# Kernel optimization log

Hardware: AMD Instinct MI355X
Metric: run time of the kernel (lower is better)

The kernel has to match this reference:

```python
import jax, jax.numpy as jnp
import numpy as np

# dims
R, K, N, V = 2, 3, 16384, 256          # r_len, num feat keys, nodes, raw feat dim
E, L, VE = 1, 8, 128                   # num extra keys, extra seq len, extra raw dim
LK, OUT = 1, 64                        # num label keys, out_feats (num classes)
IN, HID = 256, 512                     # in_feats, hidden
C = K + E + LK                         # num_channels for grouped conv / LayerNorm
LN_EPS = 1e-5


def _xav(key, shape, fan_in, fan_out):
    s = np.sqrt(2.0 / (fan_in + fan_out)).astype(np.float32)
    return jax.random.normal(key, shape, dtype=jnp.float32) * s


def setup_inputs() -> dict:
    key = jax.random.key(0)
    ks = jax.random.split(key, 16)
    inp = {}
    # forward args (dict-of-tensor structures flattened to stacked arrays in sorted-key order)
    inp["raw_feats"] = jax.random.normal(ks[0], (R, K, N, V), dtype=jnp.float32)
    inp["extra_feats"] = jax.random.normal(ks[1], (R, E, N, L, VE), dtype=jnp.float32)
    inp["label_feats"] = jax.random.normal(ks[2], (R, LK, N, OUT), dtype=jnp.float32)
    # per-relation embedding tables (original: uniform(-0.5,0.5); scaled for numeric tameness)
    inp["feat_emb"] = jax.random.uniform(ks[3], (R, K, V, IN), minval=-0.05, maxval=0.05, dtype=jnp.float32)
    inp["extra_emb"] = jax.random.uniform(ks[4], (R, E, VE, IN), minval=-0.05, maxval=0.05, dtype=jnp.float32)
    inp["label_emb"] = jax.random.uniform(ks[5], (R, LK, OUT, IN), minval=-0.05, maxval=0.05, dtype=jnp.float32)
    # sigmoid-attention weight vectors
    inp["w_extra"] = _xav(ks[6], (E, IN), IN, 1)      # embed_weight_r_extra
    inp["w_r"] = _xav(ks[7], (R, HID), HID, 1)        # embed_weight_r
    inp["w_global"] = _xav(ks[8], (HID,), HID, 1)     # self.w
    # grouped conv1x1 stack + LayerNorm([C,HID]) + PReLU (x2)
    inp["W1"] = _xav(ks[9], (C, IN, HID), IN, HID)
    inp["b1"] = jnp.zeros((C, HID), jnp.float32)
    inp["g1"] = jnp.ones((C, HID), jnp.float32)
    inp["be1"] = jnp.zeros((C, HID), jnp.float32)
    inp["a1"] = jnp.float32(0.25)
    inp["W2"] = _xav(ks[10], (C, HID, HID), HID, HID)
    inp["b2"] = jnp.zeros((C, HID), jnp.float32)
    inp["g2"] = jnp.ones((C, HID), jnp.float32)
    inp["be2"] = jnp.zeros((C, HID), jnp.float32)
    inp["a2"] = jnp.float32(0.25)
    # FeedForwardNet (n_layers_2 = 2)
    inp["Wf1"] = _xav(ks[11], (HID, HID), HID, HID)
    inp["bf1"] = jnp.zeros((HID,), jnp.float32)
    inp["af"] = jnp.float32(0.25)
    inp["Wf2"] = _xav(ks[12], (HID, OUT), HID, OUT)
    inp["bf2"] = jnp.zeros((OUT,), jnp.float32)
    return inp


def _prelu(x, a):
    return jnp.where(x >= 0, x, a * x)


def _ln(x, g, b):
    # LayerNorm over last two dims ([C, HID]) as in nn.LayerNorm([num_channels, hidden])
    m = jnp.mean(x, axis=(-2, -1), keepdims=True)
    v = jnp.var(x, axis=(-2, -1), keepdims=True)
    return (x - m) * jax.lax.rsqrt(v + LN_EPS) * g + b


def _attn_pool(f, w):
    # f: [N, C, D], w: [D] -> softmax(sigmoid(f @ w)) over C, weighted sum -> [N, D]
    gv = jax.nn.softmax(jax.nn.sigmoid(f @ w), axis=-1)
    return jnp.einsum('ncd,nc->nd', f, gv)


def reference(raw_feats, extra_feats, label_feats, feat_emb, extra_emb, label_emb,
              w_extra, w_r, w_global, W1, b1, g1, be1, a1, W2, b2, g2, be2, a2,
              Wf1, bf1, af, Wf2, bf2):
    outs = []
    for r in range(R):  # small fixed ensemble loop (structurally distinct params)
        mapped = jnp.einsum('knv,kvd->nkd', raw_feats[r], feat_emb[r])        # [N,K,IN]
        me = jnp.einsum('enlv,evd->enld', extra_feats[r], extra_emb[r])       # [E,N,L,IN]
        extra_out = jax.vmap(_attn_pool)(me, w_extra)                          # [E,N,IN]
        ml = jnp.einsum('knc,kcd->nkd', label_feats[r], label_emb[r])         # [N,LK,IN]
        feats = jnp.concatenate([mapped, jnp.moveaxis(extra_out, 0, 1), ml], axis=1)  # [N,C,IN]
        x = jnp.einsum('ncm,cmh->nch', feats, W1) + b1                         # grouped conv1x1
        x = _prelu(_ln(x, g1, be1), a1)
        x = jnp.einsum('nch,chk->nck', x, W2) + b2
        x = _prelu(_ln(x, g2, be2), a2)
        outs.append(_attn_pool(x, w_r[r]))                                     # [N,HID]
    h = jnp.stack(outs, axis=1)                                                # [N,R,HID]
    final = _attn_pool(h, w_global)                                            # [N,HID]
    y = _prelu(final @ Wf1 + bf1, af)
    return y @ Wf2 + bf2
```

## Files before the change

### kernel.cpp

```cpp
#include <hip/hip_runtime.h>


typedef unsigned short bf16_t;
using ushort8v = __attribute__((ext_vector_type(8))) unsigned short;
using bf16x8   = __attribute__((ext_vector_type(8))) __bf16;
using f32x4    = __attribute__((ext_vector_type(4))) float;

#define WAITV(N) asm volatile("s_waitcnt vmcnt(%0)" :: "n"(N) : "memory")
#define WAITL0() asm volatile("s_waitcnt lgkmcnt(0)" ::: "memory")

__device__ __forceinline__ float bf2f(bf16_t u) {
    return __uint_as_float(((unsigned int)u) << 16);
}
__device__ __forceinline__ bf16_t f2bf(float f) {
    unsigned int u = __float_as_uint(f);
    u += 0x7FFFu + ((u >> 16) & 1u);
    return (bf16_t)(u >> 16);
}
__device__ __forceinline__ float ld1(const void* p, long i, int dt) {
    return dt ? bf2f(((const bf16_t*)p)[i]) : ((const float*)p)[i];
}
__device__ __forceinline__ float4 ld4(const void* p, long i, int dt) {
    if (dt) {
        ushort4 v = *(const ushort4*)((const bf16_t*)p + i);
        return make_float4(bf2f(v.x), bf2f(v.y), bf2f(v.z), bf2f(v.w));
    }
    return *(const float4*)((const float*)p + i);
}
__device__ __forceinline__ ushort8v ld8bf(const void* p, long i, int dt) {
    if (dt) return *(const ushort8v*)((const bf16_t*)p + i);
    const float* f = (const float*)p + i;
    float4 a = *(const float4*)f, b = *(const float4*)(f + 4);
    ushort8v r;
    r[0] = f2bf(a.x); r[1] = f2bf(a.y); r[2] = f2bf(a.z); r[3] = f2bf(a.w);
    r[4] = f2bf(b.x); r[5] = f2bf(b.y); r[6] = f2bf(b.z); r[7] = f2bf(b.w);
    return r;
}
__device__ __forceinline__ float decode_scalar(const void* p, int isbf) {
    if (!isbf) return *(const float*)p;
    unsigned int u = *(const unsigned int*)p;
    if ((u & 0xFFFFu) == 0u) return __uint_as_float(u);
    return bf2f((bf16_t)(u & 0xFFFFu));
}
__device__ __forceinline__ float wave_reduce(float v) {
#pragma unroll
    for (int o = 32; o > 0; o >>= 1) v += __shfl_down(v, o, 64);
    return v;
}
__device__ __forceinline__ void gl_lds16(const void* g, void* l) {
    __builtin_amdgcn_global_load_lds(
        (const __attribute__((address_space(1))) void*)g,
        (__attribute__((address_space(3))) void*)l, 16, 0, 0);
}

__global__ void detect_k(const unsigned int* __restrict__ w, long nwords,
                         int* __restrict__ flag)
{
    const int lane = threadIdx.x;
    long idx = (long)lane * 997 + 13;
    if (idx >= nwords) idx = lane % (nwords > 0 ? nwords : 1);
    unsigned int word = w[idx];
    int e = (word >> 7) & 0xFF;
    int vote = (e >= 110 && e <= 134) ? 1 : 0;
    unsigned long long m = __ballot(vote);
    if (lane == 0) *flag = (__popcll(m) >= 32) ? 1 : 0;
}

__global__ __launch_bounds__(256) void transT_k(
    const void* __restrict__ in, long inoff, long sInZ, int Kd, int Nd,
    bf16_t* __restrict__ out, long outoff, long sOutZ,
    const int* __restrict__ flag)
{
    const int isbf = *flag;
    const long z = blockIdx.z;
    long idx = (long)blockIdx.x * 256 + threadIdx.x;
    if (idx >= (long)Kd * Nd) return;
    int k = (int)(idx / Nd), n = (int)(idx % Nd);
    out[outoff + z * sOutZ + (long)n * Kd + k] =
        f2bf(ld1(in, inoff + z * sInZ + idx, isbf));
}

__global__ __launch_bounds__(256) void fold_gemmT_k(
    const void* __restrict__ A, long aoff, long sAz, int lda,
    const void* __restrict__ B, long boff, long sBz, int ldb,
    bf16_t* __restrict__ CT, long coff, long sCz, int ldcT,
    int K, const int* __restrict__ flag)
{
    const int isbf = *flag;
    __shared__ __align__(16) float As[16][68];
    __shared__ __align__(16) float Bs[16][68];
    const int z = blockIdx.z, t = threadIdx.x;
    const int tx = t & 15, ty = t >> 4;
    const int am = t >> 2, ak = (t & 3) << 2;
    const int bn = tx << 2;
    const long aBase = aoff + z * sAz + (long)(blockIdx.y * 64 + am) * lda + ak;
    const long bBase = boff + z * sBz + (long)ty * ldb + blockIdx.x * 64 + bn;
    float acc[4][4] = {};
    for (int k0 = 0; k0 < K; k0 += 16) {
        float4 av = ld4(A, aBase + k0, isbf);
        float4 bv = ld4(B, bBase + (long)k0 * ldb, isbf);
        __syncthreads();
        As[ak + 0][am] = av.x; As[ak + 1][am] = av.y;
        As[ak + 2][am] = av.z; As[ak + 3][am] = av.w;
        *(float4*)&Bs[ty][bn] = bv;
        __syncthreads();
#pragma unroll
        for (int k = 0; k < 16; k++) {
            float4 a4 = *(const float4*)&As[k][ty << 2];
            float4 b4 = *(const float4*)&Bs[k][tx << 2];
            float ar[4] = {a4.x, a4.y, a4.z, a4.w};
            float br[4] = {b4.x, b4.y, b4.z, b4.w};
#pragma unroll
            for (int i = 0; i < 4; i++)
#pragma unroll
                for (int j = 0; j < 4; j++) acc[i][j] += ar[i] * br[j];
        }
    }
    const int cm = blockIdx.y * 64 + (ty << 2);
    const int cn = blockIdx.x * 64 + (tx << 2);
#pragma unroll
    for (int i = 0; i < 4; i++)
#pragma unroll
        for (int j = 0; j < 4; j++)
            CT[coff + z * sCz + (long)(cn + j) * ldcT + (cm + i)] = f2bf(acc[i][j]);
}

template <int BN_, int WNW_, int MODE, int CD>
__global__ __launch_bounds__(256) void mgemm(
    const void* __restrict__ A, int adt, long aoff, long sA1, long sA2, int lda,
    const bf16_t* __restrict__ BT, long boff, long sB1, long sB2,
    void* __restrict__ C, long coff, long sC1, long sC2, int ldc,
    const void* __restrict__ bias, long biasoff, long sBi1, long sBi2,
    const void* __restrict__ alpha_ptr, int K, int zdiv,
    const int* __restrict__ flag)
{
    constexpr int NJ = WNW_ / 16;
    constexpr int BROUNDS = BN_ / 64;
    const int isbf = *flag;
    const int adt_ = (adt == 2) ? isbf : adt;
    const int cdt = (CD == 2) ? isbf : 1;

    __shared__ __align__(16) unsigned short As[3][128 * 32];
    __shared__ __align__(16) unsigned short Bs[3][BN_ * 32];

    const int t = threadIdx.x;
    const int lane = t & 63, w = t >> 6;
    const int quad = lane >> 4, r16 = lane & 15;
    const int wy = w >> 1, wx = w & 1;
    const int z = blockIdx.z;
    const int zq = z / zdiv, zr = z % zdiv;
    const long blockM = (long)blockIdx.y * 128;
    const int  blockN = blockIdx.x * BN_;

    f32x4 acc[4][NJ];
    const f32x4 zero4 = {0.f, 0.f, 0.f, 0.f};
#pragma unroll
    for (int i = 0; i < 4; i++)
#pragma unroll
        for (int j = 0; j < NJ; j++) acc[i][j] = zero4;

    const long aBase = aoff + zq * sA1 + zr * sA2;
    const long bBase = boff + zq * sB1 + zr * sB2;

    const bool fastA = (adt_ == 1);
    const bf16_t* Abf = (const bf16_t*)A;

    auto STAGE = [&](int buf, int ti) {
        const int k0 = ti << 5;
        if (fastA) {
#pragma unroll
            for (int c = 0; c < 2; c++) {
                const int lin = c * 256 + t;
                const int m = lin >> 2, kq = (lin & 3) * 8;
                gl_lds16(Abf + aBase + (blockM + m) * (long)lda + k0 + kq,
                         &As[buf][(size_t)(c * 256 + w * 64) * 8]);
            }
        } else {
            ushort8v av[2];
#pragma unroll
            for (int c = 0; c < 2; c++) {
                const int lin = c * 256 + t;
                const int m = lin >> 2, kq = (lin & 3) * 8;
                av[c] = ld8bf(A, aBase + (blockM + m) * (long)lda + k0 + kq, 0);
            }
#pragma unroll
            for (int c = 0; c < 2; c++)
                *(ushort8v*)&As[buf][(size_t)(c * 256 + t) * 8] = av[c];
        }
#pragma unroll
        for (int c = 0; c < BROUNDS; c++) {
            const int lin = c * 256 + t;
            const int n = lin >> 2, kq = (lin & 3) * 8;
            gl_lds16(BT + bBase + (long)(blockN + n) * K + k0 + kq,
                     &Bs[buf][(size_t)(c * 256 + w * 64) * 8]);
        }
    };

    const int nt = K >> 5;
    STAGE(0, 0);
    if (nt > 1) STAGE(1, 1);

    int cur = 0;
    for (int ti = 0; ti < nt; ++ti) {
        WAITL0();
        if (fastA) {
            if (ti + 1 < nt) WAITV(2 + BROUNDS); else WAITV(0);
        } else {
            if (ti + 1 < nt) WAITV(BROUNDS);     else WAITV(0);
        }
        __builtin_amdgcn_s_barrier();
        __builtin_amdgcn_sched_barrier(0);

        if (ti + 2 < nt) {
            int sb = cur + 2; if (sb >= 3) sb -= 3;
            STAGE(sb, ti + 2);
        }

        bf16x8 af[4], bfr[NJ];
#pragma unroll
        for (int i = 0; i < 4; i++) {
            int m = wy * 64 + i * 16 + r16;
            af[i] = __builtin_bit_cast(bf16x8,
                        *(const ushort8v*)&As[cur][m * 32 + quad * 8]);
        }
#pragma unroll
        for (int j = 0; j < NJ; j++) {
            int n = wx * WNW_ + j * 16 + r16;
            bfr[j] = __builtin_bit_cast(bf16x8,
                        *(const ushort8v*)&Bs[cur][n * 32 + quad * 8]);
        }
#pragma unroll
        for (int i = 0; i < 4; i++)
#pragma unroll
            for (int j = 0; j < NJ; j++)
                acc[i][j] = __builtin_amdgcn_mfma_f32_16x16x32_bf16(
                    af[i], bfr[j], acc[i][j], 0, 0, 0);

        cur = (cur == 2) ? 0 : cur + 1;
    }

    const float alpha = (MODE == 2) ? decode_scalar(alpha_ptr, isbf) : 0.f;
    const long cBase = coff + zq * sC1 + zr * sC2;
#pragma unroll
    for (int j = 0; j < NJ; j++) {
        const int n = blockN + wx * WNW_ + j * 16 + r16;
        const float bz = (MODE >= 1)
            ? ld1(bias, biasoff + zq * sBi1 + zr * sBi2 + n, isbf) : 0.f;
#pragma unroll
        for (int i = 0; i < 4; i++) {
            const long m0 = blockM + wy * 64 + i * 16 + quad * 4;
#pragma unroll
            for (int rg = 0; rg < 4; rg++) {
                float v = acc[i][j][rg] + bz;
                if (MODE == 2) v = (v >= 0.f) ? v : alpha * v;
                const long off = cBase + (m0 + rg) * (long)ldc + n;
                if (cdt) ((bf16_t*)C)[off] = f2bf(v);
                else     ((float*)C)[off] = v;
            }
        }
    }
}

__global__ __launch_bounds__(256) void pool_extra_k(
    const bf16_t* __restrict__ ME, long sMEz, const void* __restrict__ wx,
    float* __restrict__ EO, long sEOz, const int* __restrict__ flag)
{
    const int isbf = *flag;
    const int n = blockIdx.x, t = threadIdx.x;
    const bf16_t* base = ME + blockIdx.y * sMEz + (long)n * 2048;
    float v[8];
#pragma unroll
    for (int l = 0; l < 8; l++) v[l] = bf2f(base[l * 256 + t]);
    const float w = ld1(wx, t, isbf);
    __shared__ float red[8][4];
    const int lane = t & 63, wid = t >> 6;
#pragma unroll
    for (int l = 0; l < 8; l++) {
        float pr = wave_reduce(v[l] * w);
        if (lane == 0) red[l][wid] = pr;
    }
    __syncthreads();
    float gv[8], ssum = 0.f;
#pragma unroll
    for (int l = 0; l < 8; l++) {
        float sc = red[l][0] + red[l][1] + red[l][2] + red[l][3];
        float sg = 1.f / (1.f + expf(-sc));
        float e = expf(sg);
        gv[l] = e; ssum += e;
    }
    const float inv = 1.f / ssum;
    float o = 0.f;
#pragma unroll
    for (int l = 0; l < 8; l++) o += gv[l] * inv * v[l];
    EO[blockIdx.y * sEOz + (long)n * 256 + t] = o;
}

__global__ __launch_bounds__(256) void ln1_k(
    bf16_t* __restrict__ X, const void* __restrict__ g,
    const void* __restrict__ be, const void* __restrict__ alpha_ptr,
    const int* __restrict__ flag)
{
    const int isbf = *flag;
    const int n = blockIdx.x, t = threadIdx.x;
    bf16_t* row = X + (long)n * 2560;
    float v[10], s = 0.f, sq = 0.f;
#pragma unroll
    for (int i = 0; i < 10; i++) {
        float x = bf2f(row[i * 256 + t]);
        v[i] = x; s += x; sq += x * x;
    }
    __shared__ float redS[4], redQ[4];
    const int lane = t & 63, wid = t >> 6;
    float ws_ = wave_reduce(s), wq = wave_reduce(sq);
    if (lane == 0) { redS[wid] = ws_; redQ[wid] = wq; }
    __syncthreads();
    const float S = redS[0] + redS[1] + redS[2] + redS[3];
    const float Q = redQ[0] + redQ[1] + redQ[2] + redQ[3];
    const float mean = S * (1.f / 2560.f);
    const float rstd = rsqrtf(fmaxf(Q * (1.f / 2560.f) - mean * mean, 0.f) + 1e-5f);
    const float alpha = decode_scalar(alpha_ptr, isbf);
#pragma unroll
    for (int i = 0; i < 10; i++) {
        int e = i * 256 + t;
        float y = (v[i] - mean) * rstd * ld1(g, e, isbf) + ld1(be, e, isbf);
        row[e] = f2bf((y >= 0.f) ? y : alpha * y);
    }
}

__global__ __launch_bounds__(256) void ln2_pool_k(
    const bf16_t* __restrict__ X, long sXz, const void* __restrict__ g,
    const void* __restrict__ be, const void* __restrict__ alpha_ptr,
    const void* __restrict__ wr,
    bf16_t* __restrict__ H, const int* __restrict__ flag)
{
    const int isbf = *flag;
    const int n = blockIdx.x, t = threadIdx.x, rr = blockIdx.y;
    const bf16_t* row = X + rr * sXz + (long)n * 2560;
    float v[5][2], s = 0.f, sq = 0.f;
#pragma unroll
    for (int c = 0; c < 5; c++)
#pragma unroll
        for (int hi = 0; hi < 2; hi++) {
            float x = bf2f(row[c * 512 + hi * 256 + t]);
            v[c][hi] = x; s += x; sq += x * x;
        }
    __shared__ float redS[4], redQ[4];
    const int lane = t & 63, wid = t >> 6;
    float ws_ = wave_reduce(s), wq = wave_reduce(sq);
    if (lane == 0) { redS[wid] = ws_; redQ[wid] = wq; }
    __syncthreads();
    const float S = redS[0] + redS[1] + redS[2] + redS[3];
    const float Q = redQ[0] + redQ[1] + redQ[2] + redQ[3];
    const float mean = S * (1.f / 2560.f);
    const float rstd = rsqrtf(fmaxf(Q * (1.f / 2560.f) - mean * mean, 0.f) + 1e-5f);
    const float alpha = decode_scalar(alpha_ptr, isbf);
    const float w0 = ld1(wr, (long)rr * 512 + t, isbf);
    const float w1 = ld1(wr, (long)rr * 512 + t + 256, isbf);
    float p[5];
#pragma unroll
    for (int c = 0; c < 5; c++) {
        p[c] = 0.f;
#pragma unroll
        for (int hi = 0; hi < 2; hi++) {
            int e = c * 512 + hi * 256 + t;
            float y = (v[c][hi] - mean) * rstd * ld1(g, e, isbf) + ld1(be, e, isbf);
            y = (y >= 0.f) ? y : alpha * y;
            v[c][hi] = y;
            p[c] += y * (hi ? w1 : w0);
        }
    }
    __shared__ float redP[5][4];
#pragma unroll
    for (int c = 0; c < 5; c++) {
        float pr = wave_reduce(p[c]);
        if (lane == 0) redP[c][wid] = pr;
    }
    __syncthreads();
    float gv[5], ssum = 0.f;
#pragma unroll
    for (int c = 0; c < 5; c++) {
        float sc = redP[c][0] + redP[c][1] + redP[c][2] + redP[c][3];
        float sg = 1.f / (1.f + expf(-sc));
        float e = expf(sg);
        gv[c] = e; ssum += e;
    }
    const float inv = 1.f / ssum;
#pragma unroll
    for (int hi = 0; hi < 2; hi++) {
        float o = 0.f;
#pragma unroll
        for (int c = 0; c < 5; c++) o += gv[c] * inv * v[c][hi];
        H[(long)n * 1024 + rr * 512 + hi * 256 + t] = f2bf(o);
    }
}

__global__ __launch_bounds__(256) void gpool_k(
    const bf16_t* __restrict__ H, const void* __restrict__ wg,
    bf16_t* __restrict__ F, const int* __restrict__ flag)
{
    const int isbf = *flag;
    const int n = blockIdx.x, t = threadIdx.x;
    const bf16_t* base = H + (long)n * 1024;
    const float w0 = ld1(wg, t, isbf), w1 = ld1(wg, t + 256, isbf);
    float v[2][2], p[2];
#pragma unroll
    for (int r = 0; r < 2; r++) {
        v[r][0] = bf2f(base[r * 512 + t]);
        v[r][1] = bf2f(base[r * 512 + 256 + t]);
        p[r] = v[r][0] * w0 + v[r][1] * w1;
    }
    __shared__ float red[2][4];
    const int lane = t & 63, wid = t >> 6;
#pragma unroll
    for (int r = 0; r < 2; r++) {
        float pr = wave_reduce(p[r]);
        if (lane == 0) red[r][wid] = pr;
    }
    __syncthreads();
    float gv[2], ssum = 0.f;
#pragma unroll
    for (int r = 0; r < 2; r++) {
        float sc = red[r][0] + red[r][1] + red[r][2] + red[r][3];
        float sg = 1.f / (1.f + expf(-sc));
        float e = expf(sg);
        gv[r] = e; ssum += e;
    }
    const float inv = 1.f / ssum;
#pragma unroll
    for (int hi = 0; hi < 2; hi++) {
        F[(long)n * 512 + hi * 256 + t] =
            f2bf((gv[0] * v[0][hi] + gv[1] * v[1][hi]) * inv);
    }
}

extern "C" void kernel_launch(void* const* d_in, const int* in_sizes, int n_in,
                              void* d_out, int out_size, void* d_ws, size_t ws_size,
                              hipStream_t stream)
{
    const void* raw   = d_in[0];
    const void* extra = d_in[1];
    const void* lbl   = d_in[2];
    const void* femb  = d_in[3];
    const void* eemb  = d_in[4];
    const void* lemb  = d_in[5];
    const void* wx    = d_in[6];
    const void* wr    = d_in[7];
    const void* wg    = d_in[8];
    const void* W1    = d_in[9];
    const void* b1    = d_in[10];
    const void* g1    = d_in[11];
    const void* be1   = d_in[12];
    const void* a1    = d_in[13];
    const void* W2    = d_in[14];
    const void* b2    = d_in[15];
    const void* g2    = d_in[16];
    const void* be2   = d_in[17];
    const void* a2    = d_in[18];
    const void* Wf1   = d_in[19];
    const void* bf1   = d_in[20];
    const void* af    = d_in[21];
    const void* Wf2   = d_in[22];
    const void* bf2b  = d_in[23];

    int*    flag  = (int*)d_ws;
    bf16_t* MfT   = (bf16_t*)((char*)d_ws + 256);
    bf16_t* MlT   = MfT + 786432;
    bf16_t* W1c3T = MlT + 65536;
    bf16_t* W2T   = W1c3T + 131072;
    bf16_t* Wf1T  = W2T + 1310720;
    bf16_t* Wf2T  = Wf1T + 262144;
    bf16_t* eT    = Wf2T + 32768;
    char*   arena = (char*)(eT + 65536);
    const size_t fixedBytes = 256 + 2654208 * 2;

    int Nc = 16384;
    while (Nc > 128 && fixedBytes + (size_t)Nc * 24576 > ws_size) Nc >>= 1;
    const int NCH = 16384 / Nc;

    bf16_t* x1  = (bf16_t*)arena;
    bf16_t* x2  = (bf16_t*)(arena + (size_t)Nc * 10240);
    float*  eo  = (float*) (arena + (size_t)Nc * 20480);
    bf16_t* hbc = (bf16_t*)(arena + (size_t)Nc * 22528);
    bf16_t* mec = x1;
    bf16_t* fin = x2;
    bf16_t* zb  = x2 + (size_t)Nc * 512;

    dim3 blk(256);

    detect_k<<<1, 64, 0, stream>>>((const unsigned int*)raw,
                                   (long)in_sizes[0] / 2, flag);

    transT_k<<<dim3(1024, 1, 5), blk, 0, stream>>>(W2, 0, 262144, 512, 512,
                                                   W2T, 0, 262144, flag);
    transT_k<<<dim3(512, 1, 1), blk, 0, stream>>>(W1, 3L * 131072, 0, 256, 512,
                                                  W1c3T, 0, 0, flag);
    transT_k<<<dim3(1024, 1, 1), blk, 0, stream>>>(Wf1, 0, 0, 512, 512,
                                                   Wf1T, 0, 0, flag);
    transT_k<<<dim3(128, 1, 1), blk, 0, stream>>>(Wf2, 0, 0, 512, 64,
                                                  Wf2T, 0, 0, flag);
    transT_k<<<dim3(128, 1, 2), blk, 0, stream>>>(eemb, 0, 32768, 128, 256,
                                                  eT, 0, 32768, flag);

    for (int r = 0; r < 2; r++) {
        fold_gemmT_k<<<dim3(8, 4, 3), blk, 0, stream>>>(
            femb, (long)r * 196608, 65536, 256,
            W1, 0, 131072, 512,
            MfT, (long)r * 393216, 131072, 256, 256, flag);
    }
    fold_gemmT_k<<<dim3(8, 1, 2), blk, 0, stream>>>(
        lemb, 0, 16384, 256,
        W1, 4L * 131072, 0, 512,
        MlT, 0, 32768, 64, 256, flag);

    for (int c = 0; c < NCH; c++) {
        const long n0 = (long)c * Nc;

        mgemm<128, 64, 0, 1><<<dim3(2, Nc * 8 / 128, 2), blk, 0, stream>>>(
            extra, 2, n0 * 1024, 16777216, 0, 128,
            eT, 0, 32768, 0,
            mec, 0, (long)Nc * 8 * 256, 0, 256,
            nullptr, 0, 0, 0, nullptr, 128, 1, flag);
        pool_extra_k<<<dim3(Nc, 2), blk, 0, stream>>>(
            mec, (long)Nc * 8 * 256, wx, eo, (long)Nc * 256, flag);

        mgemm<128, 64, 1, 1><<<dim3(4, Nc / 128, 6), blk, 0, stream>>>(
            raw, 2, n0 * 256, 12582912, 4194304, 256,
            MfT, 0, 393216, 131072,
            x1, 0, (long)Nc * 2560, 512, 2560,
            b1, 0, 0, 512, nullptr, 256, 3, flag);
        mgemm<128, 64, 1, 1><<<dim3(4, Nc / 128, 2), blk, 0, stream>>>(
            eo, 0, 0, (long)Nc * 256, 0, 256,
            W1c3T, 0, 0, 0,
            x1, 3L * 512, (long)Nc * 2560, 0, 2560,
            b1, 3L * 512, 0, 0, nullptr, 256, 1, flag);
        mgemm<128, 64, 1, 1><<<dim3(4, Nc / 128, 2), blk, 0, stream>>>(
            lbl, 2, n0 * 64, 1048576, 0, 64,
            MlT, 0, 32768, 0,
            x1, 4L * 512, (long)Nc * 2560, 0, 2560,
            b1, 4L * 512, 0, 0, nullptr, 64, 1, flag);

        ln1_k<<<2 * Nc, blk, 0, stream>>>(x1, g1, be1, a1, flag);

        mgemm<128, 64, 1, 1><<<dim3(4, Nc / 128, 10), blk, 0, stream>>>(
            x1, 1, 0, (long)Nc * 2560, 512, 2560,
            W2T, 0, 0, 262144,
            x2, 0, (long)Nc * 2560, 512, 2560,
            b2, 0, 0, 512, nullptr, 512, 5, flag);

        ln2_pool_k<<<dim3(Nc, 2), blk, 0, stream>>>(
            x2, (long)Nc * 2560, g2, be2, a2, wr, hbc, flag);

        gpool_k<<<Nc, blk, 0, stream>>>(hbc, wg, fin, flag);

        mgemm<128, 64, 2, 1><<<dim3(4, Nc / 128, 1), blk, 0, stream>>>(
            fin, 1, 0, 0, 0, 512,
            Wf1T, 0, 0, 0,
            zb, 0, 0, 0, 512,
            bf1, 0, 0, 0, af, 512, 1, flag);
        mgemm<64, 32, 1, 2><<<dim3(1, Nc / 128, 1), blk, 0, stream>>>(
            zb, 1, 0, 0, 0, 512,
            Wf2T, 0, 0, 0,
            d_out, n0 * 64, 0, 0, 64,
            bf2b, 0, 0, 0, nullptr, 512, 1, flag);
    }
}
```

Baseline: 1.032 ms.

## Fuse extra-feature GEMM with attention pooling and apply LN1 inside W2 GEMM

The extra-feature embedding GEMM and its sigmoid-attention pooling are merged into one MFMA kernel (egp_k) that pools in registers, so the [N,8,256] intermediate is never written to or re-read from memory. LayerNorm1 plus PReLU is split: a small kernel writes only per-row mean and rstd, and the W2 grouped GEMM normalizes and activates A tiles as it loads them. This removes the read-modify-write pass over x1. In exchange, the LN-fused GEMM drops its async global-to-LDS fast path for A and does extra per-element arithmetic and gamma/beta loads in the staging loop, and egp_k uses small 64-row tiles.

```diff
diff --git a/kernel.cpp b/kernel.cpp
--- a/kernel.cpp
+++ b/kernel.cpp
@@ -125,13 +125,15 @@
             CT[coff + z * sCz + (long)(cn + j) * ldcT + (cm + i)] = f2bf(acc[i][j]);
 }
 
-template <int BN_, int WNW_, int MODE, int CD>
+template <int BN_, int WNW_, int MODE, int CD, int LNA>
 __global__ __launch_bounds__(256) void mgemm(
     const void* __restrict__ A, int adt, long aoff, long sA1, long sA2, int lda,
     const bf16_t* __restrict__ BT, long boff, long sB1, long sB2,
     void* __restrict__ C, long coff, long sC1, long sC2, int ldc,
     const void* __restrict__ bias, long biasoff, long sBi1, long sBi2,
     const void* __restrict__ alpha_ptr, int K, int zdiv,
+    const void* __restrict__ lnstats, const void* __restrict__ lng,
+    const void* __restrict__ lnbe, const void* __restrict__ lnal,
     const int* __restrict__ flag)
 {
     constexpr int NJ = WNW_ / 16;
@@ -162,8 +164,18 @@
     const long aBase = aoff + zq * sA1 + zr * sA2;
     const long bBase = boff + zq * sB1 + zr * sB2;
 
-    const bool fastA = (adt_ == 1);
+    const bool fastA = (adt_ == 1) && !LNA;
     const bf16_t* Abf = (const bf16_t*)A;
+
+    float mu0 = 0.f, rs0 = 0.f, mu1 = 0.f, rs1 = 0.f, lnalpha = 0.f;
+    if (LNA) {
+        const float* st = (const float*)lnstats;
+        const long Ntot = (long)gridDim.y * 128;
+        const long r0 = zq * Ntot + blockM + (t >> 2);
+        mu0 = st[r0 * 2];        rs0 = st[r0 * 2 + 1];
+        mu1 = st[(r0 + 64) * 2]; rs1 = st[(r0 + 64) * 2 + 1];
+        lnalpha = decode_scalar(lnal, isbf);
+    }
 
     auto STAGE = [&](int buf, int ti) {
         const int k0 = ti << 5;
@@ -181,7 +193,29 @@
             for (int c = 0; c < 2; c++) {
                 const int lin = c * 256 + t;
                 const int m = lin >> 2, kq = (lin & 3) * 8;
-                av[c] = ld8bf(A, aBase + (blockM + m) * (long)lda + k0 + kq, 0);
+                if (LNA) {
+                    ushort8v x = *(const ushort8v*)(
+                        Abf + aBase + (blockM + m) * (long)lda + k0 + kq);
+                    const long kc = (long)zr * sA2 + k0 + kq;
+                    float4 ga = ld4(lng,  kc,     isbf);
+                    float4 gb = ld4(lng,  kc + 4, isbf);
+                    float4 ba = ld4(lnbe, kc,     isbf);
+                    float4 bb = ld4(lnbe, kc + 4, isbf);
+                    const float mu = c ? mu1 : mu0, rs = c ? rs1 : rs0;
+                    float gr[8] = {ga.x, ga.y, ga.z, ga.w, gb.x, gb.y, gb.z, gb.w};
+                    float br[8] = {ba.x, ba.y, ba.z, ba.w, bb.x, bb.y, bb.z, bb.w};
+                    ushort8v o;
+#pragma unroll
+                    for (int e = 0; e < 8; e++) {
+                        float y = (bf2f(x[e]) - mu) * rs;
+                        y = y * gr[e] + br[e];
+                        y = (y >= 0.f) ? y : lnalpha * y;
+                        o[e] = f2bf(y);
+                    }
+                    av[c] = o;
+                } else {
+                    av[c] = ld8bf(A, aBase + (blockM + m) * (long)lda + k0 + kq, 0);
+                }
             }
 #pragma unroll
             for (int c = 0; c < 2; c++)
@@ -261,69 +295,150 @@
     }
 }
 
-__global__ __launch_bounds__(256) void pool_extra_k(
-    const bf16_t* __restrict__ ME, long sMEz, const void* __restrict__ wx,
-    float* __restrict__ EO, long sEOz, const int* __restrict__ flag)
+__global__ __launch_bounds__(256) void egp_k(
+    const void* __restrict__ extra, long aoff, long sEz,
+    const bf16_t* __restrict__ eT, long sBz,
+    const void* __restrict__ wxp,
+    float* __restrict__ EO, long sEOz,
+    const int* __restrict__ flag)
 {
     const int isbf = *flag;
+    __shared__ __align__(16) unsigned short As2[64 * 32];
+    __shared__ __align__(16) unsigned short Bs2[256 * 32];
+    __shared__ float dotl[64][4];
+    __shared__ float el[64];
+    __shared__ float gwl[64];
+
+    const int t = threadIdx.x;
+    const int lane = t & 63, w = t >> 6;
+    const int quad = lane >> 4, r16 = lane & 15;
+    const long rowBase = (long)blockIdx.y * 64;
+    const int z = blockIdx.z;
+
+    f32x4 acc[4][4];
+    const f32x4 zero4 = {0.f, 0.f, 0.f, 0.f};
+#pragma unroll
+    for (int i = 0; i < 4; i++)
+#pragma unroll
+        for (int j = 0; j < 4; j++) acc[i][j] = zero4;
+
+    const long aBase = aoff + (long)z * sEz;
+    const long bBase = (long)z * sBz;
+
+    for (int k0 = 0; k0 < 128; k0 += 32) {
+        ushort8v av = ld8bf(extra,
+            aBase + (rowBase + (t >> 2)) * 128 + k0 + (t & 3) * 8, isbf);
+        __syncthreads();
+        *(ushort8v*)&As2[t * 8] = av;
+#pragma unroll
+        for (int c = 0; c < 4; c++) {
+            const int lin = c * 256 + t;
+            const int n = lin >> 2, kq = (lin & 3) * 8;
+            gl_lds16(eT + bBase + (long)n * 128 + k0 + kq,
+                     &Bs2[(size_t)(c * 256 + w * 64) * 8]);
+        }
+        __syncthreads();
+
+        bf16x8 af[4], bfr[4];
+#pragma unroll
+        for (int i = 0; i < 4; i++) {
+            int m = i * 16 + r16;
+            af[i] = __builtin_bit_cast(bf16x8,
+                        *(const ushort8v*)&As2[m * 32 + quad * 8]);
+        }
+#pragma unroll
+        for (int j = 0; j < 4; j++) {
+            int n = w * 64 + j * 16 + r16;
+            bfr[j] = __builtin_bit_cast(bf16x8,
+                        *(const ushort8v*)&Bs2[n * 32 + quad * 8]);
+        }
+#pragma unroll
+        for (int i = 0; i < 4; i++)
+#pragma unroll
+            for (int j = 0; j < 4; j++)
+                acc[i][j] = __builtin_amdgcn_mfma_f32_16x16x32_bf16(
+                    af[i], bfr[j], acc[i][j], 0, 0, 0);
+    }
+
+    float wv[4];
+#pragma unroll
+    for (int j = 0; j < 4; j++) wv[j] = ld1(wxp, w * 64 + j * 16 + r16, isbf);
+
+#pragma unroll
+    for (int i = 0; i < 4; i++) {
+#pragma unroll
+        for (int rg = 0; rg < 4; rg++) {
+            float d = acc[i][0][rg] * wv[0] + acc[i][1][rg] * wv[1]
+                    + acc[i][2][rg] * wv[2] + acc[i][3][rg] * wv[3];
+            d += __shfl_xor(d, 1, 64);
+            d += __shfl_xor(d, 2, 64);
+            d += __shfl_xor(d, 4, 64);
+            d += __shfl_xor(d, 8, 64);
+            if (r16 == 0) dotl[i * 16 + quad * 4 + rg][w] = d;
+        }
+    }
+    __syncthreads();
+    if (t < 64) {
+        float s = dotl[t][0] + dotl[t][1] + dotl[t][2] + dotl[t][3];
+        float sg = 1.f / (1.f + expf(-s));
+        el[t] = expf(sg);
+    }
+    __syncthreads();
+    if (t < 64) {
+        const int nb = t & ~7;
+        float S = 0.f;
+#pragma unroll
+        for (int l = 0; l < 8; l++) S += el[nb + l];
+        gwl[t] = el[t] / S;
+    }
+    __syncthreads();
+
+#pragma unroll
+    for (int i = 0; i < 4; i++) {
+        const int node = i * 2 + (quad >> 1);
+        float gw[4];
+#pragma unroll
+        for (int rg = 0; rg < 4; rg++) gw[rg] = gwl[i * 16 + quad * 4 + rg];
+#pragma unroll
+        for (int j = 0; j < 4; j++) {
+            float ts = gw[0] * acc[i][j][0] + gw[1] * acc[i][j][1]
+                     + gw[2] * acc[i][j][2] + gw[3] * acc[i][j][3];
+            ts += __shfl_xor(ts, 16, 64);
+            if ((quad & 1) == 0) {
+                const long ng = (long)blockIdx.y * 8 + node;
+                EO[(long)z * sEOz + ng * 256 + w * 64 + j * 16 + r16] = ts;
+            }
+        }
+    }
+}
+
+__global__ __launch_bounds__(256) void ln1_stats_k(
+    const bf16_t* __restrict__ X, float* __restrict__ st)
+{
     const int n = blockIdx.x, t = threadIdx.x;
-    const bf16_t* base = ME + blockIdx.y * sMEz + (long)n * 2048;
-    float v[8];
-#pragma unroll
-    for (int l = 0; l < 8; l++) v[l] = bf2f(base[l * 256 + t]);
-    const float w = ld1(wx, t, isbf);
-    __shared__ float red[8][4];
-    const int lane = t & 63, wid = t >> 6;
-#pragma unroll
-    for (int l = 0; l < 8; l++) {
-        float pr = wave_reduce(v[l] * w);
-        if (lane == 0) red[l][wid] = pr;
-    }
-    __syncthreads();
-    float gv[8], ssum = 0.f;
-#pragma unroll
-    for (int l = 0; l < 8; l++) {
-        float sc = red[l][0] + red[l][1] + red[l][2] + red[l][3];
-        float sg = 1.f / (1.f + expf(-sc));
-        float e = expf(sg);
-        gv[l] = e; ssum += e;
-    }
-    const float inv = 1.f / ssum;
-    float o = 0.f;
-#pragma unroll
-    for (int l = 0; l < 8; l++) o += gv[l] * inv * v[l];
-    EO[blockIdx.y * sEOz + (long)n * 256 + t] = o;
-}
-
-__global__ __launch_bounds__(256) void ln1_k(
-    bf16_t* __restrict__ X, const void* __restrict__ g,
-    const void* __restrict__ be, const void* __restrict__ alpha_ptr,
-    const int* __restrict__ flag)
-{
-    const int isbf = *flag;
-    const int n = blockIdx.x, t = threadIdx.x;
-    bf16_t* row = X + (long)n * 2560;
-    float v[10], s = 0.f, sq = 0.f;
-#pragma unroll
-    for (int i = 0; i < 10; i++) {
-        float x = bf2f(row[i * 256 + t]);
-        v[i] = x; s += x; sq += x * x;
+    const bf16_t* row = X + (long)n * 2560;
+    float s = 0.f, q = 0.f;
+    ushort8v a = *(const ushort8v*)(row + t * 8);
+#pragma unroll
+    for (int e = 0; e < 8; e++) { float f = bf2f(a[e]); s += f; q += f * f; }
+    if (t < 64) {
+        ushort8v b = *(const ushort8v*)(row + 2048 + t * 8);
+#pragma unroll
+        for (int e = 0; e < 8; e++) { float f = bf2f(b[e]); s += f; q += f * f; }
     }
     __shared__ float redS[4], redQ[4];
     const int lane = t & 63, wid = t >> 6;
-    float ws_ = wave_reduce(s), wq = wave_reduce(sq);
+    float ws_ = wave_reduce(s), wq = wave_reduce(q);
     if (lane == 0) { redS[wid] = ws_; redQ[wid] = wq; }
     __syncthreads();
-    const float S = redS[0] + redS[1] + redS[2] + redS[3];
-    const float Q = redQ[0] + redQ[1] + redQ[2] + redQ[3];
-    const float mean = S * (1.f / 2560.f);
-    const float rstd = rsqrtf(fmaxf(Q * (1.f / 2560.f) - mean * mean, 0.f) + 1e-5f);
-    const float alpha = decode_scalar(alpha_ptr, isbf);
-#pragma unroll
-    for (int i = 0; i < 10; i++) {
-        int e = i * 256 + t;
-        float y = (v[i] - mean) * rstd * ld1(g, e, isbf) + ld1(be, e, isbf);
-        row[e] = f2bf((y >= 0.f) ? y : alpha * y);
+    if (t == 0) {
+        const float S = redS[0] + redS[1] + redS[2] + redS[3];
+        const float Q = redQ[0] + redQ[1] + redQ[2] + redQ[3];
+        const float mean = S * (1.f / 2560.f);
+        const float rstd =
+            rsqrtf(fmaxf(Q * (1.f / 2560.f) - mean * mean, 0.f) + 1e-5f);
+        st[(long)n * 2]     = mean;
+        st[(long)n * 2 + 1] = rstd;
     }
 }
 
@@ -474,14 +589,14 @@
     const size_t fixedBytes = 256 + 2654208 * 2;
 
     int Nc = 16384;
-    while (Nc > 128 && fixedBytes + (size_t)Nc * 24576 > ws_size) Nc >>= 1;
+    while (Nc > 128 && fixedBytes + (size_t)Nc * 24592 > ws_size) Nc >>= 1;
     const int NCH = 16384 / Nc;
 
-    bf16_t* x1  = (bf16_t*)arena;
-    bf16_t* x2  = (bf16_t*)(arena + (size_t)Nc * 10240);
-    float*  eo  = (float*) (arena + (size_t)Nc * 20480);
-    bf16_t* hbc = (bf16_t*)(arena + (size_t)Nc * 22528);
-    bf16_t* mec = x1;
+    bf16_t* x1    = (bf16_t*)arena;
+    bf16_t* x2    = (bf16_t*)(arena + (size_t)Nc * 10240);
+    float*  eo    = (float*) (arena + (size_t)Nc * 20480);
+    bf16_t* hbc   = (bf16_t*)(arena + (size_t)Nc * 22528);
+    float*  stats = (float*) (arena + (size_t)Nc * 24576);
     bf16_t* fin = x2;
     bf16_t* zb  = x2 + (size_t)Nc * 512;
 
@@ -515,52 +630,54 @@
     for (int c = 0; c < NCH; c++) {
         const long n0 = (long)c * Nc;
 
-        mgemm<128, 64, 0, 1><<<dim3(2, Nc * 8 / 128, 2), blk, 0, stream>>>(
-            extra, 2, n0 * 1024, 16777216, 0, 128,
-            eT, 0, 32768, 0,
-            mec, 0, (long)Nc * 8 * 256, 0, 256,
-            nullptr, 0, 0, 0, nullptr, 128, 1, flag);
-        pool_extra_k<<<dim3(Nc, 2), blk, 0, stream>>>(
-            mec, (long)Nc * 8 * 256, wx, eo, (long)Nc * 256, flag);
-
-        mgemm<128, 64, 1, 1><<<dim3(4, Nc / 128, 6), blk, 0, stream>>>(
+        egp_k<<<dim3(1, Nc / 8, 2), blk, 0, stream>>>(
+            extra, n0 * 1024, 16777216, eT, 32768, wx,
+            eo, (long)Nc * 256, flag);
+
+        mgemm<128, 64, 1, 1, 0><<<dim3(4, Nc / 128, 6), blk, 0, stream>>>(
             raw, 2, n0 * 256, 12582912, 4194304, 256,
             MfT, 0, 393216, 131072,
             x1, 0, (long)Nc * 2560, 512, 2560,
-            b1, 0, 0, 512, nullptr, 256, 3, flag);
-        mgemm<128, 64, 1, 1><<<dim3(4, Nc / 128, 2), blk, 0, stream>>>(
+            b1, 0, 0, 512, nullptr, 256, 3,
+            nullptr, nullptr, nullptr, nullptr, flag);
+        mgemm<128, 64, 1, 1, 0><<<dim3(4, Nc / 128, 2), blk, 0, stream>>>(
             eo, 0, 0, (long)Nc * 256, 0, 256,
             W1c3T, 0, 0, 0,
             x1, 3L * 512, (long)Nc * 2560, 0, 2560,
-            b1, 3L * 512, 0, 0, nullptr, 256, 1, flag);
-        mgemm<128, 64, 1, 1><<<dim3(4, Nc / 128, 2), blk, 0, stream>>>(
+            b1, 3L * 512, 0, 0, nullptr, 256, 1,
+            nullptr, nullptr, nullptr, nullptr, flag);
+        mgemm<128, 64, 1, 1, 0><<<dim3(4, Nc / 128, 2), blk, 0, stream>>>(
             lbl, 2, n0 * 64, 1048576, 0, 64,
             MlT, 0, 32768, 0,
             x1, 4L * 512, (long)Nc * 2560, 0, 2560,
-            b1, 4L * 512, 0, 0, nullptr, 64, 1, flag);
-
-        ln1_k<<<2 * Nc, blk, 0, stream>>>(x1, g1, be1, a1, flag);
-
-        mgemm<128, 64, 1, 1><<<dim3(4, Nc / 128, 10), blk, 0, stream>>>(
+            b1, 4L * 512, 0, 0, nullptr, 64, 1,
+            nullptr, nullptr, nullptr, nullptr, flag);
+
+        ln1_stats_k<<<2 * Nc, blk, 0, stream>>>(x1, stats);
+
+        mgemm<128, 64, 1, 1, 1><<<dim3(4, Nc / 128, 10), blk, 0, stream>>>(
             x1, 1, 0, (long)Nc * 2560, 512, 2560,
             W2T, 0, 0, 262144,
             x2, 0, (long)Nc * 2560, 512, 2560,
-            b2, 0, 0, 512, nullptr, 512, 5, flag);
+            b2, 0, 0, 512, nullptr, 512, 5,
+            stats, g1, be1, a1, flag);
 
         ln2_pool_k<<<dim3(Nc, 2), blk, 0, stream>>>(
             x2, (long)Nc * 2560, g2, be2, a2, wr, hbc, flag);
 
         gpool_k<<<Nc, blk, 0, stream>>>(hbc, wg, fin, flag);
 
-        mgemm<128, 64, 2, 1><<<dim3(4, Nc / 128, 1), blk, 0, stream>>>(
+        mgemm<128, 64, 2, 1, 0><<<dim3(4, Nc / 128, 1), blk, 0, stream>>>(
             fin, 1, 0, 0, 0, 512,
             Wf1T, 0, 0, 0,
             zb, 0, 0, 0, 512,
-            bf1, 0, 0, 0, af, 512, 1, flag);
-        mgemm<64, 32, 1, 2><<<dim3(1, Nc / 128, 1), blk, 0, stream>>>(
+            bf1, 0, 0, 0, af, 512, 1,
+            nullptr, nullptr, nullptr, nullptr, flag);
+        mgemm<64, 32, 1, 2, 0><<<dim3(1, Nc / 128, 1), blk, 0, stream>>>(
             zb, 1, 0, 0, 0, 512,
             Wf2T, 0, 0, 0,
             d_out, n0 * 64, 0, 0, 64,
-            bf2b, 0, 0, 0, nullptr, 512, 1, flag);
-    }
-}
+            bf2b, 0, 0, 0, nullptr, 512, 1,
+            nullptr, nullptr, nullptr, nullptr, flag);
+    }
+}
```

New measurement: 948.7 us. 8.1% less time.
